# Kernel tuning notes

Hardware: AMD Instinct MI355X
Metric: run time of the kernel (lower is better)

Reference implementation:

```python
import jax, jax.numpy as jnp
import numpy as np

B, S, D_IN, UNITS = 8, 2048, 512, 512


def _glorot(key, fan_in, fan_out):
    limit = np.sqrt(6.0 / (fan_in + fan_out)).astype(np.float32)
    return jax.random.uniform(key, (fan_in, fan_out), jnp.float32, -limit, limit)


def setup_inputs() -> dict:
    key = jax.random.key(0)
    kq, kwq, kwv, kwk = jax.random.split(key, 4)
    return {
        "query": jax.random.normal(kq, (B, S, D_IN), jnp.float32),
        "Wq": _glorot(kwq, D_IN, UNITS),   # W_query conv1d k=1, no bias
        "Wv": _glorot(kwv, D_IN, UNITS),   # W_value conv1d k=1, no bias
        "Wk": _glorot(kwk, D_IN, UNITS),   # W_key   conv1d k=1, no bias
    }


def reference(query, Wq, Wv, Wk):
    # Pointwise causal Conv1D(kernel=1, no bias) with sigmoid activation == sigmoid(x @ W)
    q = jax.nn.sigmoid(jnp.einsum('bsd,du->bsu', query, Wq))   # W_query(query)
    k = jax.nn.sigmoid(jnp.einsum('bsd,du->bsu', query, Wv))   # W_value(key=query)
    v = jax.nn.sigmoid(jnp.einsum('bsd,du->bsu', query, Wk))   # W_key(value=query)

    d_in = query.shape[-1]  # scaling uses value's input feature dim, not units
    score = jnp.einsum('bqu,bku->bqk', q, k) / jnp.sqrt(jnp.float32(d_in))  # [B,S,S]

    # Mask: upper triangle INCLUDING diagonal is -inf (strictly-causal, no self)
    s = score.shape[1]
    masked = jnp.where(jnp.triu(jnp.ones((s, s), bool)), -jnp.inf, score)

    # Row 0 is fully masked -> replaced by zeros; rows 1: softmax over j < i
    rest = jax.nn.softmax(masked[:, 1:, :], axis=-1)
    attn = jnp.concatenate([jnp.zeros((score.shape[0], 1, s), score.dtype), rest], axis=1)

    return jnp.einsum('bqk,bku->bqu', attn, v)
```

## Files before the change

### kernel.cpp

```cpp
#include <hip/hip_runtime.h>
#include <stdint.h>


typedef __attribute__((ext_vector_type(4))) float f32x4;
typedef __attribute__((ext_vector_type(8))) short short8;
typedef __attribute__((ext_vector_type(4))) short short4b;

__device__ __forceinline__ short f2bf(float f) {
    union { float f; uint32_t u; } v; v.f = f;
    uint32_t r = (v.u + 0x7FFFu + ((v.u >> 16) & 1u)) >> 16;
    return (short)r;
}
__device__ __forceinline__ float bf2f(short s) {
    union { uint32_t u; float f; } v; v.u = ((uint32_t)(uint16_t)s) << 16; return v.f;
}
__device__ __forceinline__ float sigm(float x) { return 1.0f / (1.0f + __expf(-x)); }

__device__ __forceinline__ void gload_lds16(const void* g, void* l) {
    __builtin_amdgcn_global_load_lds(
        (const __attribute__((address_space(1))) void*)g,
        (__attribute__((address_space(3))) void*)l, 16, 0, 0);
}

__global__ __launch_bounds__(256) void prep_weights(
    const float* __restrict__ Wq, const float* __restrict__ Wv, const float* __restrict__ Wk,
    short* __restrict__ Wt)
{
    __shared__ float T[64 * 68];
    int bid = blockIdx.x;
    int w = bid >> 6;
    int tile = bid & 63;
    int n0 = (tile & 7) * 64;
    int k0 = (tile >> 3) * 64;
    const float* W = (w == 0) ? Wq : (w == 1) ? Wv : Wk;
    int t = threadIdx.x;
    int tr = t >> 4, tc = t & 15;
    for (int rr = 0; rr < 4; ++rr) {
        int row = rr * 16 + tr;
        float4 v = *reinterpret_cast<const float4*>(&W[(size_t)(k0 + row) * 512 + n0 + tc * 4]);
        T[row * 68 + tc * 4 + 0] = v.x;
        T[row * 68 + tc * 4 + 1] = v.y;
        T[row * 68 + tc * 4 + 2] = v.z;
        T[row * 68 + tc * 4 + 3] = v.w;
    }
    __syncthreads();
    for (int wr = 0; wr < 4; ++wr) {
        int nl = wr * 16 + tr;
        short4b o;
        for (int i = 0; i < 4; ++i) o[i] = f2bf(T[(tc * 4 + i) * 68 + nl]);
        *reinterpret_cast<short4b*>(&Wt[((size_t)(w * 512 + n0 + nl)) * 512 + k0 + tc * 4]) = o;
    }
}

__global__ __launch_bounds__(256) void qkv_gemm(
    const float* __restrict__ X,
    const short* __restrict__ Wt,
    short* __restrict__ Qb, short* __restrict__ Kb, short* __restrict__ VtG)
{
    __shared__ short SMEM[128 * 128];
    short* As = SMEM;
    short* Bs = SMEM + 128 * 64;

    int bx = blockIdx.x;
    int mt = bx & 127;
    int y = bx >> 7;
    int w = y >> 2, nt = y & 3;
    int m0 = mt * 128, n0 = nt * 128;

    int tid = threadIdx.x;
    int wid = tid >> 6, lane = tid & 63;
    int wr = wid >> 1, wc = wid & 1;
    int ln = lane & 15, hi = lane >> 4;

    f32x4 acc[4][4];
    for (int i = 0; i < 4; ++i) for (int j = 0; j < 4; ++j) acc[i][j] = {0.f, 0.f, 0.f, 0.f};

    const short* WtW = Wt + (size_t)w * 512 * 512;

    for (int ko = 0; ko < 8; ++ko) {
        int k0 = ko * 64;
        __syncthreads();
        for (int j = 0; j < 8; ++j) {
            int c = j * 256 + tid;
            int row = c >> 4, col4 = c & 15;
            float4 v = *reinterpret_cast<const float4*>(&X[(size_t)(m0 + row) * 512 + k0 + col4 * 4]);
            short4b s;
            s[0] = f2bf(v.x); s[1] = f2bf(v.y); s[2] = f2bf(v.z); s[3] = f2bf(v.w);
            *reinterpret_cast<short4b*>(&As[row * 64 + ((col4 * 4) ^ ((row & 7) << 3))]) = s;
        }
        for (int j = 0; j < 4; ++j) {
            int c = j * 256 + tid;
            int row = c >> 3, col8 = c & 7;
            short8 v = *reinterpret_cast<const short8*>(&WtW[(size_t)(n0 + row) * 512 + k0 + col8 * 8]);
            *reinterpret_cast<short8*>(&Bs[row * 64 + ((col8 * 8) ^ ((row & 7) << 3))]) = v;
        }
        __syncthreads();
        for (int kk = 0; kk < 2; ++kk) {
            int kof = kk * 32 + hi * 8;
            int sw = (ln & 7) << 3;
            short8 af[4], bf[4];
            for (int mf = 0; mf < 4; ++mf)
                af[mf] = *reinterpret_cast<const short8*>(&As[(wr * 64 + mf * 16 + ln) * 64 + (kof ^ sw)]);
            for (int nf = 0; nf < 4; ++nf)
                bf[nf] = *reinterpret_cast<const short8*>(&Bs[(wc * 64 + nf * 16 + ln) * 64 + (kof ^ sw)]);
            for (int mf = 0; mf < 4; ++mf)
                for (int nf = 0; nf < 4; ++nf)
                    acc[mf][nf] = __builtin_amdgcn_mfma_f32_16x16x32_bf16(af[mf], bf[nf], acc[mf][nf], 0, 0, 0);
        }
    }
    __syncthreads();

    if (w < 2) {
        short* O = (w == 0) ? Qb : Kb;
        for (int mf = 0; mf < 4; ++mf)
            for (int nf = 0; nf < 4; ++nf)
                for (int j = 0; j < 4; ++j) {
                    int row = m0 + wr * 64 + mf * 16 + hi * 4 + j;
                    int col = n0 + wc * 64 + nf * 16 + ln;
                    O[(size_t)row * 512 + col] = f2bf(sigm(acc[mf][nf][j]));
                }
    } else {
        for (int mf = 0; mf < 4; ++mf)
            for (int nf = 0; nf < 4; ++nf)
                for (int j = 0; j < 4; ++j) {
                    int ml = wr * 64 + mf * 16 + hi * 4 + j;
                    int nl = wc * 64 + nf * 16 + ln;
                    SMEM[nl * 128 + (ml ^ ((nl & 7) << 3))] = f2bf(sigm(acc[mf][nf][j]));
                }
        __syncthreads();
        int bb = m0 >> 11;
        int s0 = m0 & 2047;
        int d = tid >> 1, h = tid & 1;
        for (int i = 0; i < 8; ++i) {
            int s8 = h * 64 + i * 8;
            short8 v = *reinterpret_cast<const short8*>(&SMEM[d * 128 + (s8 ^ ((d & 7) << 3))]);
            *reinterpret_cast<short8*>(&VtG[((size_t)(bb * 512 + n0 + d)) * 2048 + s0 + s8]) = v;
        }
    }
}

__global__ __launch_bounds__(256) void score_pass(
    const short* __restrict__ Qb, const short* __restrict__ Kb,
    short* __restrict__ Pc, float* __restrict__ Dpart)
{
    __shared__ short SMEM[128 * 128];
    __shared__ float psum[2][128];
    short* As = SMEM;
    short* Bs = SMEM + 128 * 64;

    const float scale = 0.044194173824159216f;

    int bid = blockIdx.x;
    int b = bid & 7;
    int idx = bid >> 3;
    int ti = 0;
    while ((ti + 1) * (ti + 2) / 2 <= idx) ++ti;
    int tj = idx - ti * (ti + 1) / 2;
    int m0 = ti * 128, n0 = tj * 128;

    int tid = threadIdx.x;
    int w = tid >> 6, lane = tid & 63;
    int wr = w >> 1, wc = w & 1;
    int ln = lane & 15, hi = lane >> 4;

    const short* Qsrc = Qb + (size_t)b * 2048 * 512 + (size_t)m0 * 512;
    const short* Ksrc = Kb + (size_t)b * 2048 * 512 + (size_t)n0 * 512;

    f32x4 acc[4][4];
#pragma unroll
    for (int i = 0; i < 4; ++i)
#pragma unroll
        for (int j = 0; j < 4; ++j) acc[i][j] = {0.f, 0.f, 0.f, 0.f};

    for (int ko = 0; ko < 8; ++ko) {
        int k0 = ko * 64;
#pragma unroll
        for (int j = 0; j < 4; ++j) {
            int r = w * 8 + j * 32 + (lane >> 3);
            int sc = ((lane & 7) * 8) ^ ((r & 7) << 3);
            gload_lds16(Qsrc + (size_t)r * 512 + k0 + sc, &As[(w * 8 + j * 32) * 64]);
        }
#pragma unroll
        for (int j = 0; j < 4; ++j) {
            int r = w * 8 + j * 32 + (lane >> 3);
            int sc = ((lane & 7) * 8) ^ ((r & 7) << 3);
            gload_lds16(Ksrc + (size_t)r * 512 + k0 + sc, &Bs[(w * 8 + j * 32) * 64]);
        }
        __syncthreads();
#pragma unroll
        for (int kk = 0; kk < 2; ++kk) {
            int kof = kk * 32 + hi * 8;
            int sw = (ln & 7) << 3;
            short8 af[4], bf[4];
#pragma unroll
            for (int mf = 0; mf < 4; ++mf)
                af[mf] = *reinterpret_cast<const short8*>(&As[(wr * 64 + mf * 16 + ln) * 64 + (kof ^ sw)]);
#pragma unroll
            for (int nf = 0; nf < 4; ++nf)
                bf[nf] = *reinterpret_cast<const short8*>(&Bs[(wc * 64 + nf * 16 + ln) * 64 + (kof ^ sw)]);
#pragma unroll
            for (int mf = 0; mf < 4; ++mf)
#pragma unroll
                for (int nf = 0; nf < 4; ++nf)
                    acc[mf][nf] = __builtin_amdgcn_mfma_f32_16x16x32_bf16(af[mf], bf[nf], acc[mf][nf], 0, 0, 0);
        }
        __syncthreads();
    }

    short* Ptile = Pc + (size_t)(b * 136 + idx) * 128 * 128;
#pragma unroll
    for (int mf = 0; mf < 4; ++mf) {
        float rs[4] = {0.f, 0.f, 0.f, 0.f};
#pragma unroll
        for (int nf = 0; nf < 4; ++nf)
#pragma unroll
            for (int j = 0; j < 4; ++j) {
                int rl = wr * 64 + mf * 16 + hi * 4 + j;
                int cl = wc * 64 + nf * 16 + ln;
                int irow = m0 + rl, jcol = n0 + cl;
                float p = (jcol < irow) ? __expf(acc[mf][nf][j] * scale) : 0.f;
                short hs = f2bf(p);
                Ptile[(size_t)rl * 128 + cl] = hs;
                rs[j] += bf2f(hs);
            }
#pragma unroll
        for (int j = 0; j < 4; ++j) {
            float s = rs[j];
            s += __shfl_xor(s, 1);
            s += __shfl_xor(s, 2);
            s += __shfl_xor(s, 4);
            s += __shfl_xor(s, 8);
            if (ln == 0) psum[wc][wr * 64 + mf * 16 + hi * 4 + j] = s;
        }
    }
    __syncthreads();
    if (tid < 128)
        Dpart[((size_t)b * 16 + tj) * 2048 + m0 + tid] = psum[0][tid] + psum[1][tid];
}

__global__ __launch_bounds__(256) void pv_pass(
    const short* __restrict__ Pc, const short* __restrict__ VtG,
    const float* __restrict__ Dpart, float* __restrict__ Out)
{
    __shared__ short SMEM[128 * 64 + 64 * 64];
    __shared__ float dnm[128];
    short* As = SMEM;
    short* Bs = SMEM + 128 * 64;

    int bid = blockIdx.x;
    int b = bid & 7;
    int rr = bid >> 3;
    int grp = rr >> 5, off = rr & 31;
    int ti = (grp & 1) ? (15 - (off >> 1)) : (off >> 1);
    int colhalf = 2 * grp + (off & 1);
    int m0 = ti * 128, n0 = colhalf * 64;

    int tid = threadIdx.x;
    int w = tid >> 6, lane = tid & 63;
    int wr = w >> 1, wc = w & 1;
    int ln = lane & 15, hi = lane >> 4;

    if (tid < 128) {
        float s = 0.f;
        for (int tj = 0; tj <= ti; ++tj)
            s += Dpart[((size_t)b * 16 + tj) * 2048 + m0 + tid];
        int gi = m0 + tid;
        dnm[tid] = (gi == 0) ? 0.f : 1.0f / s;
    }

    const short* Ptiles = Pc + (size_t)(b * 136 + ti * (ti + 1) / 2) * 128 * 128;
    const short* Vsrc = VtG + (size_t)b * 512 * 2048 + (size_t)n0 * 2048;

    f32x4 acc[4][2];
#pragma unroll
    for (int i = 0; i < 4; ++i)
#pragma unroll
        for (int j = 0; j < 2; ++j) acc[i][j] = {0.f, 0.f, 0.f, 0.f};

    for (int ks = 0; ks < 2 * (ti + 1); ++ks) {
        int tj = ks >> 1;
        int j0 = (ks & 1) * 64;
        const short* Pt = Ptiles + (size_t)tj * 128 * 128;
#pragma unroll
        for (int j = 0; j < 4; ++j) {
            int r = w * 8 + j * 32 + (lane >> 3);
            int sc = ((lane & 7) * 8) ^ ((r & 7) << 3);
            gload_lds16(Pt + (size_t)r * 128 + j0 + sc, &As[(w * 8 + j * 32) * 64]);
        }
#pragma unroll
        for (int j = 0; j < 2; ++j) {
            int r = w * 8 + j * 32 + (lane >> 3);
            int sc = ((lane & 7) * 8) ^ ((r & 7) << 3);
            gload_lds16(Vsrc + (size_t)r * 2048 + tj * 128 + j0 + sc, &Bs[(w * 8 + j * 32) * 64]);
        }
        __syncthreads();
#pragma unroll
        for (int kk = 0; kk < 2; ++kk) {
            int kof = kk * 32 + hi * 8;
            int sw = (ln & 7) << 3;
            short8 af[4], bf[2];
#pragma unroll
            for (int mf = 0; mf < 4; ++mf)
                af[mf] = *reinterpret_cast<const short8*>(&As[(wr * 64 + mf * 16 + ln) * 64 + (kof ^ sw)]);
#pragma unroll
            for (int nf = 0; nf < 2; ++nf)
                bf[nf] = *reinterpret_cast<const short8*>(&Bs[(wc * 32 + nf * 16 + ln) * 64 + (kof ^ sw)]);
#pragma unroll
            for (int mf = 0; mf < 4; ++mf)
#pragma unroll
                for (int nf = 0; nf < 2; ++nf)
                    acc[mf][nf] = __builtin_amdgcn_mfma_f32_16x16x32_bf16(af[mf], bf[nf], acc[mf][nf], 0, 0, 0);
        }
        __syncthreads();
    }

#pragma unroll
    for (int mf = 0; mf < 4; ++mf)
#pragma unroll
        for (int j = 0; j < 4; ++j) {
            int rl = wr * 64 + mf * 16 + hi * 4 + j;
            float rd = dnm[rl];
            float* orow = Out + ((size_t)b * 2048 + m0 + rl) * 512 + n0 + wc * 32 + ln;
#pragma unroll
            for (int nf = 0; nf < 2; ++nf)
                orow[nf * 16] = acc[mf][nf][j] * rd;
        }
}

extern "C" void kernel_launch(void* const* d_in, const int* in_sizes, int n_in,
                              void* d_out, int out_size, void* d_ws, size_t ws_size,
                              hipStream_t stream) {
    const float* X  = (const float*)d_in[0];
    const float* Wq = (const float*)d_in[1];
    const float* Wv = (const float*)d_in[2];
    const float* Wk = (const float*)d_in[3];
    float* Out = (float*)d_out;

    char* ws = (char*)d_ws;
    const size_t WT_BYTES  = (size_t)3 * 512 * 512 * 2;
    const size_t MAT_BYTES = (size_t)16384 * 512 * 2;
    const size_t PC_BYTES  = (size_t)8 * 136 * 128 * 128 * 2;
    short* Wt = (short*)ws;
    short* Qb = (short*)(ws + WT_BYTES);
    short* Kb = (short*)(ws + WT_BYTES + MAT_BYTES);
    short* Vt = (short*)(ws + WT_BYTES + 2 * MAT_BYTES);
    short* Pc = (short*)(ws + WT_BYTES + 3 * MAT_BYTES);
    float* Dp = (float*)(ws + WT_BYTES + 3 * MAT_BYTES + PC_BYTES);

    prep_weights<<<192, 256, 0, stream>>>(Wq, Wv, Wk, Wt);
    qkv_gemm<<<1536, 256, 0, stream>>>(X, Wt, Qb, Kb, Vt);
    score_pass<<<1088, 256, 0, stream>>>(Qb, Kb, Pc, Dp);
    pv_pass<<<1024, 256, 0, stream>>>(Pc, Vt, Dp, Out);
}
```

Measured before the change: 142.0 us.

## Pre-convert X to bf16 and load GEMM tiles via direct global-to-LDS

```diff
diff --git a/kernel.cpp b/kernel.cpp
--- a/kernel.cpp
+++ b/kernel.cpp
@@ -20,6 +20,18 @@
     __builtin_amdgcn_global_load_lds(
         (const __attribute__((address_space(1))) void*)g,
         (__attribute__((address_space(3))) void*)l, 16, 0, 0);
+}
+
+__global__ __launch_bounds__(256) void convert_x(
+    const float* __restrict__ X, short* __restrict__ Xb)
+{
+    size_t i = (size_t)blockIdx.x * 256 + threadIdx.x;
+    const float4* src = reinterpret_cast<const float4*>(X) + i * 2;
+    float4 a = src[0], b = src[1];
+    short8 o;
+    o[0] = f2bf(a.x); o[1] = f2bf(a.y); o[2] = f2bf(a.z); o[3] = f2bf(a.w);
+    o[4] = f2bf(b.x); o[5] = f2bf(b.y); o[6] = f2bf(b.z); o[7] = f2bf(b.w);
+    *reinterpret_cast<short8*>(Xb + i * 8) = o;
 }
 
 __global__ __launch_bounds__(256) void prep_weights(
@@ -53,7 +65,7 @@
 }
 
 __global__ __launch_bounds__(256) void qkv_gemm(
-    const float* __restrict__ X,
+    const short* __restrict__ Xb,
     const short* __restrict__ Wt,
     short* __restrict__ Qb, short* __restrict__ Kb, short* __restrict__ VtG)
 {
@@ -68,60 +80,72 @@
     int m0 = mt * 128, n0 = nt * 128;
 
     int tid = threadIdx.x;
-    int wid = tid >> 6, lane = tid & 63;
-    int wr = wid >> 1, wc = wid & 1;
+    int wv = tid >> 6, lane = tid & 63;
+    int wr = wv >> 1, wc = wv & 1;
     int ln = lane & 15, hi = lane >> 4;
 
     f32x4 acc[4][4];
-    for (int i = 0; i < 4; ++i) for (int j = 0; j < 4; ++j) acc[i][j] = {0.f, 0.f, 0.f, 0.f};
-
-    const short* WtW = Wt + (size_t)w * 512 * 512;
+#pragma unroll
+    for (int i = 0; i < 4; ++i)
+#pragma unroll
+        for (int j = 0; j < 4; ++j) acc[i][j] = {0.f, 0.f, 0.f, 0.f};
+
+    const short* Asrc = Xb + (size_t)m0 * 512;
+    const short* Bsrc = Wt + (size_t)w * 512 * 512 + (size_t)n0 * 512;
 
     for (int ko = 0; ko < 8; ++ko) {
         int k0 = ko * 64;
-        __syncthreads();
-        for (int j = 0; j < 8; ++j) {
-            int c = j * 256 + tid;
-            int row = c >> 4, col4 = c & 15;
-            float4 v = *reinterpret_cast<const float4*>(&X[(size_t)(m0 + row) * 512 + k0 + col4 * 4]);
-            short4b s;
-            s[0] = f2bf(v.x); s[1] = f2bf(v.y); s[2] = f2bf(v.z); s[3] = f2bf(v.w);
-            *reinterpret_cast<short4b*>(&As[row * 64 + ((col4 * 4) ^ ((row & 7) << 3))]) = s;
-        }
-        for (int j = 0; j < 4; ++j) {
-            int c = j * 256 + tid;
-            int row = c >> 3, col8 = c & 7;
-            short8 v = *reinterpret_cast<const short8*>(&WtW[(size_t)(n0 + row) * 512 + k0 + col8 * 8]);
-            *reinterpret_cast<short8*>(&Bs[row * 64 + ((col8 * 8) ^ ((row & 7) << 3))]) = v;
-        }
-        __syncthreads();
+#pragma unroll
+        for (int j = 0; j < 4; ++j) {
+            int r = wv * 8 + j * 32 + (lane >> 3);
+            int sc = ((lane & 7) * 8) ^ ((r & 7) << 3);
+            gload_lds16(Asrc + (size_t)r * 512 + k0 + sc, &As[(wv * 8 + j * 32) * 64]);
+        }
+#pragma unroll
+        for (int j = 0; j < 4; ++j) {
+            int r = wv * 8 + j * 32 + (lane >> 3);
+            int sc = ((lane & 7) * 8) ^ ((r & 7) << 3);
+            gload_lds16(Bsrc + (size_t)r * 512 + k0 + sc, &Bs[(wv * 8 + j * 32) * 64]);
+        }
+        __syncthreads();
+#pragma unroll
         for (int kk = 0; kk < 2; ++kk) {
             int kof = kk * 32 + hi * 8;
             int sw = (ln & 7) << 3;
             short8 af[4], bf[4];
+#pragma unroll
             for (int mf = 0; mf < 4; ++mf)
                 af[mf] = *reinterpret_cast<const short8*>(&As[(wr * 64 + mf * 16 + ln) * 64 + (kof ^ sw)]);
+#pragma unroll
             for (int nf = 0; nf < 4; ++nf)
                 bf[nf] = *reinterpret_cast<const short8*>(&Bs[(wc * 64 + nf * 16 + ln) * 64 + (kof ^ sw)]);
-            for (int mf = 0; mf < 4; ++mf)
+#pragma unroll
+            for (int mf = 0; mf < 4; ++mf)
+#pragma unroll
                 for (int nf = 0; nf < 4; ++nf)
                     acc[mf][nf] = __builtin_amdgcn_mfma_f32_16x16x32_bf16(af[mf], bf[nf], acc[mf][nf], 0, 0, 0);
         }
-    }
-    __syncthreads();
+        __syncthreads();
+    }
 
     if (w < 2) {
         short* O = (w == 0) ? Qb : Kb;
+#pragma unroll
         for (int mf = 0; mf < 4; ++mf)
+#pragma unroll
             for (int nf = 0; nf < 4; ++nf)
+#pragma unroll
                 for (int j = 0; j < 4; ++j) {
                     int row = m0 + wr * 64 + mf * 16 + hi * 4 + j;
                     int col = n0 + wc * 64 + nf * 16 + ln;
                     O[(size_t)row * 512 + col] = f2bf(sigm(acc[mf][nf][j]));
                 }
     } else {
+#pragma unroll
         for (int mf = 0; mf < 4; ++mf)
+#pragma unroll
             for (int nf = 0; nf < 4; ++nf)
+#pragma unroll
                 for (int j = 0; j < 4; ++j) {
                     int ml = wr * 64 + mf * 16 + hi * 4 + j;
                     int nl = wc * 64 + nf * 16 + ln;
@@ -131,6 +155,7 @@
         int bb = m0 >> 11;
         int s0 = m0 & 2047;
         int d = tid >> 1, h = tid & 1;
+#pragma unroll
         for (int i = 0; i < 8; ++i) {
             int s8 = h * 64 + i * 8;
             short8 v = *reinterpret_cast<const short8*>(&SMEM[d * 128 + (s8 ^ ((d & 7) << 3))]);
@@ -345,10 +370,12 @@
     short* Kb = (short*)(ws + WT_BYTES + MAT_BYTES);
     short* Vt = (short*)(ws + WT_BYTES + 2 * MAT_BYTES);
     short* Pc = (short*)(ws + WT_BYTES + 3 * MAT_BYTES);
+    short* Xb = Pc;
     float* Dp = (float*)(ws + WT_BYTES + 3 * MAT_BYTES + PC_BYTES);
 
+    convert_x<<<4096, 256, 0, stream>>>(X, Xb);
     prep_weights<<<192, 256, 0, stream>>>(Wq, Wv, Wk, Wt);
-    qkv_gemm<<<1536, 256, 0, stream>>>(X, Wt, Qb, Kb, Vt);
+    qkv_gemm<<<1536, 256, 0, stream>>>(Xb, Wt, Qb, Kb, Vt);
     score_pass<<<1088, 256, 0, stream>>>(Qb, Kb, Pc, Dp);
     pv_pass<<<1024, 256, 0, stream>>>(Pc, Vt, Dp, Out);
 }
```

Result: faster. 137.1 us (-3.4%).
